# Optimization experiments

Hardware: AMD Instinct MI355X
Metric: run time of the kernel (lower is better)

## Reference

```python
import jax, jax.numpy as jnp
import numpy as np

IN_COUNT = 1024
OUT_COUNT = 1024
NUM_BASIS = 8
INPUT_ABS_MAX = 1.0
X_MIN = 0.0
X_MAX = 1.0
GAMMA_SCALE = 3.0
BATCH = 4096


def setup_inputs() -> dict:
    key = jax.random.key(0)
    k_x, k_c = jax.random.split(key)
    x = jax.random.normal(k_x, (BATCH, IN_COUNT), dtype=jnp.float32)
    coeffs = 0.01 * jax.random.normal(k_c, (OUT_COUNT, IN_COUNT, NUM_BASIS), dtype=jnp.float32)
    # fixed buffers
    centers_1d = jnp.linspace(X_MIN, X_MAX, NUM_BASIS)
    centers = jnp.broadcast_to(centers_1d[None, :], (IN_COUNT, NUM_BASIS)).astype(jnp.float32)
    delta = (X_MAX - X_MIN) / (NUM_BASIS - 1)
    gamma = GAMMA_SCALE / delta
    slopes = jnp.full((IN_COUNT, NUM_BASIS), gamma, dtype=jnp.float32)
    alpha = jnp.full((IN_COUNT,), (X_MAX - X_MIN) / (2.0 * INPUT_ABS_MAX), dtype=jnp.float32)
    beta = jnp.full((IN_COUNT,), 0.5 * (X_MIN + X_MAX), dtype=jnp.float32)
    return {"x": x, "coeffs": coeffs, "centers": centers, "slopes": slopes, "alpha": alpha, "beta": beta}


def reference(x, coeffs, centers, slopes, alpha, beta):
    # u: (B, in) affine transform with fixed alpha/beta
    u = alpha[None, :] * x + beta[None, :]
    # basis: (B, in, basis) = 0.5*(1+tanh(slope*(u - center)))
    basis = 0.5 * (1.0 + jnp.tanh(slopes[None, :, :] * (u[:, :, None] - centers[None, :, :])))
    # y[b,o] = sum_{i,m} coeffs[o,i,m] * basis[b,i,m]  (fused GEMM over in*basis)
    y = jnp.einsum('bim,oim->bo', basis, coeffs)
    return y
```

## Files before the change

kernel.cpp:

```cpp
#include <hip/hip_runtime.h>
#include <hip/hip_bf16.h>
#include <cstdint>
#include <cstddef>

#define BATCH 4096
#define INC   1024
#define OUTC  1024
#define NB    8
#define KDIM  (INC * NB)

#define BM 128
#define BN 128
#define BKB 128
#define SPLITS 3
#define GRID_BLOCKS ((OUTC / BN) * (BATCH / BM) * SPLITS)

#define EXPAND_BLOCKS  ((BATCH * INC) / 256)
#define QUANT_BLOCKS   OUTC
#define PREP_BLOCKS    (EXPAND_BLOCKS + QUANT_BLOCKS)

typedef int   v4i __attribute__((ext_vector_type(4)));
typedef char  v8c __attribute__((ext_vector_type(8)));
typedef short v8s __attribute__((ext_vector_type(8)));

__device__ __forceinline__ unsigned short f2bf(float f) {
  union { float f; unsigned u; } v; v.f = f;
  unsigned r = v.u + 0x7fffu + ((v.u >> 16) & 1u);
  return (unsigned short)(r >> 16);
}
__device__ __forceinline__ float bf2f(unsigned short h) {
  union { unsigned u; float f; } v; v.u = ((unsigned)h) << 16; return v.f;
}

__device__ __forceinline__ void gld16(const char* g, char* l) {
  __builtin_amdgcn_global_load_lds(
      (const __attribute__((address_space(1))) unsigned int*)g,
      (__attribute__((address_space(3))) unsigned int*)l, 16, 0, 0);
}

__global__ __launch_bounds__(256) void prep_kernel(
    const float* __restrict__ x, const float4* __restrict__ coeffs4,
    const float* __restrict__ centers, const float* __restrict__ slopes,
    const float* __restrict__ alpha, const float* __restrict__ beta,
    char* __restrict__ Ai8, int* __restrict__ Ci8i,
    float* __restrict__ maxrow, int* __restrict__ qcsum) {
  const int blk = blockIdx.x;
  const int tid = threadIdx.x;
  if (blk < EXPAND_BLOCKS) {
    const int idx = blk * 256 + tid;
    const int i = idx & (INC - 1);
    const float u = alpha[i] * x[idx] + beta[i];
    const float s0 = slopes[i * NB];
    const float c0 = centers[i * NB];
    const float c1 = centers[i * NB + 1];
    const float L2E2 = 2.8853900817779268f;
    const float a2 = L2E2 * s0;
    float e = __builtin_amdgcn_exp2f(a2 * (c0 - u));
    const float R = __builtin_amdgcn_exp2f(a2 * (c1 - c0));
    v8c q;
#pragma unroll
    for (int m = 0; m < 8; ++m) {
      float basis = __builtin_amdgcn_rcpf(1.0f + e);
      q[m] = (char)(int)rintf(basis * 254.0f - 127.0f);
      e *= R;
    }
    *(v8c*)(Ai8 + (size_t)idx * 8) = q;
  } else {
    const int o = blk - EXPAND_BLOCKS;
    const float4* row = coeffs4 + (size_t)o * (KDIM / 4);
    float4 v[8];
    float m = 0.0f;
#pragma unroll
    for (int j = 0; j < 8; ++j) {
      v[j] = row[tid + 256 * j];
      m = fmaxf(m, fmaxf(fmaxf(fabsf(v[j].x), fabsf(v[j].y)),
                         fmaxf(fabsf(v[j].z), fabsf(v[j].w))));
    }
#pragma unroll
    for (int off = 32; off; off >>= 1) m = fmaxf(m, __shfl_xor(m, off));
    __shared__ float wm[4];
    __shared__ int   wq[4];
    if ((tid & 63) == 0) wm[tid >> 6] = m;
    __syncthreads();
    const float M = fmaxf(fmaxf(fmaxf(wm[0], wm[1]), fmaxf(wm[2], wm[3])), 1e-30f);
    const float s = 127.0f / M;
    int qs = 0;
#pragma unroll
    for (int j = 0; j < 8; ++j) {
      int q0 = (int)rintf(v[j].x * s), q1 = (int)rintf(v[j].y * s);
      int q2 = (int)rintf(v[j].z * s), q3 = (int)rintf(v[j].w * s);
      Ci8i[(size_t)o * (KDIM / 4) + tid + 256 * j] =
          (q0 & 0xFF) | ((q1 & 0xFF) << 8) | ((q2 & 0xFF) << 16) | ((q3 & 0xFF) << 24);
      qs += q0 + q1 + q2 + q3;
    }
#pragma unroll
    for (int off = 32; off; off >>= 1) qs += __shfl_xor(qs, off);
    if ((tid & 63) == 0) wq[tid >> 6] = qs;
    __syncthreads();
    if (tid == 0) { maxrow[o] = M; qcsum[o] = wq[0] + wq[1] + wq[2] + wq[3]; }
  }
}

__global__ __launch_bounds__(256, 3) void gemm_kernel(
    const char* __restrict__ A, const char* __restrict__ C,
    unsigned short* __restrict__ partials) {
  __shared__ char As[BM * BKB];
  __shared__ char Bs[BN * BKB];

  const int id = (blockIdx.x & 7) * (GRID_BLOCKS / 8) + (blockIdx.x >> 3);
  const int z  = id >> 8;
  const int p  = id & 255;
  const int st = p >> 6;
  const int q  = p & 63;
  const int bx = q & 7;
  const int by = st * 8 + (q >> 3);
  const int bn0 = bx * BN;
  const int bm0 = by * BM;

  const int iters = (z == 0) ? 22 : 21;
  const int kt0   = (z == 0) ? 0 : (2816 + 2688 * (z - 1));

  const int tid  = threadIdx.x;
  const int wave = tid >> 6;
  const int lane = tid & 63;
  const int quad = lane >> 4;
  const int lm   = lane & 15;
  const int wm = (wave & 1) * 64;
  const int wn = (wave >> 1) * 64;
  unsigned short* out = partials + (size_t)z * BATCH * OUTC;

  const int r_in = lane >> 3;
  const int kg   = (lane & 7) ^ r_in;

  const char* pA[4];
  const char* pB[4];
  char* lA[4];
  char* lB[4];
#pragma unroll
  for (int j = 0; j < 4; ++j) {
    const int rb = wave * 32 + j * 8;
    pA[j] = A + (size_t)(bm0 + rb + r_in) * KDIM + kt0 + kg * 16;
    pB[j] = C + (size_t)(bn0 + rb + r_in) * KDIM + kt0 + kg * 16;
    lA[j] = As + rb * BKB;
    lB[j] = Bs + rb * BKB;
  }

  v4i acc[4][4] = {};

  for (int it = 0; it < iters; ++it) {
#pragma unroll
    for (int j = 0; j < 4; ++j) {
      gld16(pA[j], lA[j]);
      gld16(pB[j], lB[j]);
      pA[j] += BKB; pB[j] += BKB;
    }
    __syncthreads();

#pragma unroll
    for (int kp = 0; kp < 2; ++kp) {
      v4i a[4], b[4];
#pragma unroll
      for (int fm = 0; fm < 4; ++fm) {
        const int row = wm + fm * 16 + lm;
        const int kgs = (kp * 4 + quad) ^ (row & 7);
        a[fm] = *(const v4i*)(As + row * BKB + kgs * 16);
      }
#pragma unroll
      for (int fn = 0; fn < 4; ++fn) {
        const int row = wn + fn * 16 + lm;
        const int kgs = (kp * 4 + quad) ^ (row & 7);
        b[fn] = *(const v4i*)(Bs + row * BKB + kgs * 16);
      }
#pragma unroll
      for (int fm = 0; fm < 4; ++fm)
#pragma unroll
        for (int fn = 0; fn < 4; ++fn)
          acc[fm][fn] = __builtin_amdgcn_mfma_i32_16x16x64_i8(a[fm], b[fn], acc[fm][fn], 0, 0, 0);
    }
    __syncthreads();
  }

#pragma unroll
  for (int fm = 0; fm < 4; ++fm) {
    const int row0 = bm0 + wm + fm * 16 + quad * 4;
#pragma unroll
    for (int fn = 0; fn < 4; ++fn) {
      const int col = bn0 + wn + fn * 16 + lm;
#pragma unroll
      for (int r = 0; r < 4; ++r)
        out[(size_t)(row0 + r) * OUTC + col] = f2bf((float)acc[fm][fn][r]);
    }
  }
}

__global__ __launch_bounds__(256) void reduce_kernel(
    const unsigned short* __restrict__ P, const float* __restrict__ maxrow,
    const int* __restrict__ qcsum, float* __restrict__ out) {
  const size_t nel = (size_t)BATCH * OUTC;
  const size_t base = ((size_t)blockIdx.x * 256 + threadIdx.x) * 8;
  float s[8] = {};
#pragma unroll
  for (int t = 0; t < SPLITS; ++t) {
    v8s v = *(const v8s*)(P + t * nel + base);
#pragma unroll
    for (int j = 0; j < 8; ++j) s[j] += bf2f((unsigned short)v[j]);
  }
  const int o0 = (int)(base & (OUTC - 1));
  const float inv = 1.0f / 32258.0f;
#pragma unroll
  for (int j = 0; j < 8; ++j) {
    const float M = maxrow[o0 + j];
    const int   Q = qcsum[o0 + j];
    s[j] = M * (s[j] + 127.0f * (float)Q) * inv;
  }
  *(float4*)(out + base)     = float4{s[0], s[1], s[2], s[3]};
  *(float4*)(out + base + 4) = float4{s[4], s[5], s[6], s[7]};
}

extern "C" void kernel_launch(void* const* d_in, const int* in_sizes, int n_in,
                              void* d_out, int out_size, void* d_ws, size_t ws_size,
                              hipStream_t stream) {
  const float* x       = (const float*)d_in[0];
  const float* coeffs  = (const float*)d_in[1];
  const float* centers = (const float*)d_in[2];
  const float* slopes  = (const float*)d_in[3];
  const float* alpha   = (const float*)d_in[4];
  const float* beta    = (const float*)d_in[5];
  float* out = (float*)d_out;

  const size_t a_bytes    = (size_t)BATCH * KDIM;
  const size_t c_bytes    = (size_t)OUTC * KDIM;
  const size_t stat_bytes = OUTC * sizeof(float);
  const size_t qcs_bytes  = OUTC * sizeof(int);
  const size_t part_bytes = (size_t)SPLITS * BATCH * OUTC * 2;
  if (ws_size < a_bytes + c_bytes + stat_bytes + qcs_bytes + part_bytes) return;

  char*  Ai8    = (char*)d_ws;
  char*  Ci8    = Ai8 + a_bytes;
  float* maxrow = (float*)(Ci8 + c_bytes);
  int*   qcsum  = (int*)((char*)maxrow + stat_bytes);
  unsigned short* parts = (unsigned short*)((char*)qcsum + qcs_bytes);

  prep_kernel<<<PREP_BLOCKS, 256, 0, stream>>>(
      x, (const float4*)coeffs, centers, slopes, alpha, beta,
      Ai8, (int*)Ci8, maxrow, qcsum);

  gemm_kernel<<<GRID_BLOCKS, 256, 0, stream>>>(Ai8, Ci8, parts);

  reduce_kernel<<<(int)((size_t)BATCH * OUTC / 8 / 256), 256, 0, stream>>>(
      parts, maxrow, qcsum, out);
}
```

Before: 150.7 us.

## Use 256x256 double-buffered int8 GEMM tiles with 512 threads and 4 K-splits

Enlarges the GEMM tile to 256x256 with 8 waves, shrinks the K step to 64 bytes and double-buffers LDS so the next tile's global-to-LDS loads overlap the current MFMA work. It also adds s_setprio and s_barrier scheduling hints around the MFMA blocks and moves to 4 even K splits. The aim is more data reuse per LDS byte and hidden load latency. The cost is more partial-output traffic from the extra split, only 256 blocks total, and higher register pressure from 32 accumulators per wave.

```diff
diff --git a/kernel.cpp b/kernel.cpp
--- a/kernel.cpp
+++ b/kernel.cpp
@@ -9,10 +9,12 @@
 #define NB    8
 #define KDIM  (INC * NB)
 
-#define BM 128
-#define BN 128
-#define BKB 128
-#define SPLITS 3
+#define BM 256
+#define BN 256
+#define BKB 64
+#define SPLITS 4
+#define KZ (KDIM / SPLITS)
+#define KSTEPS (KZ / BKB)
 #define GRID_BLOCKS ((OUTC / BN) * (BATCH / BM) * SPLITS)
 
 #define EXPAND_BLOCKS  ((BATCH * INC) / 256)
@@ -101,87 +103,96 @@
   }
 }
 
-__global__ __launch_bounds__(256, 3) void gemm_kernel(
+__global__ __launch_bounds__(512, 2) void gemm_kernel(
     const char* __restrict__ A, const char* __restrict__ C,
     unsigned short* __restrict__ partials) {
-  __shared__ char As[BM * BKB];
-  __shared__ char Bs[BN * BKB];
+  __shared__ __align__(16) char As[2][BM * BKB];
+  __shared__ __align__(16) char Bs[2][BN * BKB];
 
   const int id = (blockIdx.x & 7) * (GRID_BLOCKS / 8) + (blockIdx.x >> 3);
-  const int z  = id >> 8;
-  const int p  = id & 255;
-  const int st = p >> 6;
-  const int q  = p & 63;
-  const int bx = q & 7;
-  const int by = st * 8 + (q >> 3);
+  const int z  = id >> 6;
+  const int p  = id & 63;
+  const int by = p >> 2;
+  const int bx = p & 3;
+  const int bm0 = by * BM;
   const int bn0 = bx * BN;
-  const int bm0 = by * BM;
-
-  const int iters = (z == 0) ? 22 : 21;
-  const int kt0   = (z == 0) ? 0 : (2816 + 2688 * (z - 1));
+  const int kt0 = z * KZ;
 
   const int tid  = threadIdx.x;
   const int wave = tid >> 6;
   const int lane = tid & 63;
   const int quad = lane >> 4;
   const int lm   = lane & 15;
-  const int wm = (wave & 1) * 64;
-  const int wn = (wave >> 1) * 64;
+  const int wm   = (wave >> 2) * 128;
+  const int wn   = (wave & 3) * 64;
+
+  const int r4 = lane >> 2;
+  const int gg = (lane & 3) ^ ((lane >> 3) & 3);
+
+  const char* pA0 = A + (size_t)(bm0 + wave * 32 + r4) * KDIM + kt0 + gg * 16;
+  const char* pB0 = C + (size_t)(bn0 + wave * 32 + r4) * KDIM + kt0 + gg * 16;
+  const int lo = wave * 32 * BKB;
+
+  v4i acc[8][4] = {};
+  const int kx = (quad ^ ((lm >> 1) & 3)) * 16;
+
+#define STAGE(sl)                                                        \
+  {                                                                      \
+    _Pragma("unroll")                                                    \
+    for (int j = 0; j < 2; ++j) {                                        \
+      gld16(pA0 + (size_t)j * (16 * KDIM), As[sl] + lo + j * (16 * BKB));\
+      gld16(pB0 + (size_t)j * (16 * KDIM), Bs[sl] + lo + j * (16 * BKB));\
+    }                                                                    \
+    pA0 += BKB; pB0 += BKB;                                              \
+  }
+
+  STAGE(0);
+  __syncthreads();
+
+  for (int t = 0; t < KSTEPS; ++t) {
+    const int cur = t & 1;
+
+    if (t + 1 < KSTEPS) STAGE(cur ^ 1);
+
+    const char* cA = As[cur];
+    const char* cB = Bs[cur];
+    v4i a[4], b[4];
+
+#pragma unroll
+    for (int f = 0; f < 4; ++f)
+      a[f] = *(const v4i*)(cA + (wm + f * 16 + lm) * BKB + kx);
+#pragma unroll
+    for (int f = 0; f < 4; ++f)
+      b[f] = *(const v4i*)(cB + (wn + f * 16 + lm) * BKB + kx);
+    __builtin_amdgcn_s_barrier();
+    __builtin_amdgcn_s_setprio(1);
+#pragma unroll
+    for (int fm = 0; fm < 4; ++fm)
+#pragma unroll
+      for (int fn = 0; fn < 4; ++fn)
+        acc[fm][fn] = __builtin_amdgcn_mfma_i32_16x16x64_i8(a[fm], b[fn], acc[fm][fn], 0, 0, 0);
+    __builtin_amdgcn_s_setprio(0);
+    __builtin_amdgcn_s_barrier();
+
+#pragma unroll
+    for (int f = 0; f < 4; ++f)
+      a[f] = *(const v4i*)(cA + (wm + (f + 4) * 16 + lm) * BKB + kx);
+    __builtin_amdgcn_s_barrier();
+    __builtin_amdgcn_s_setprio(1);
+#pragma unroll
+    for (int fm = 0; fm < 4; ++fm)
+#pragma unroll
+      for (int fn = 0; fn < 4; ++fn)
+        acc[fm + 4][fn] = __builtin_amdgcn_mfma_i32_16x16x64_i8(a[fm], b[fn], acc[fm + 4][fn], 0, 0, 0);
+    __builtin_amdgcn_s_setprio(0);
+
+    __syncthreads();
+  }
+#undef STAGE
+
   unsigned short* out = partials + (size_t)z * BATCH * OUTC;
-
-  const int r_in = lane >> 3;
-  const int kg   = (lane & 7) ^ r_in;
-
-  const char* pA[4];
-  const char* pB[4];
-  char* lA[4];
-  char* lB[4];
-#pragma unroll
-  for (int j = 0; j < 4; ++j) {
-    const int rb = wave * 32 + j * 8;
-    pA[j] = A + (size_t)(bm0 + rb + r_in) * KDIM + kt0 + kg * 16;
-    pB[j] = C + (size_t)(bn0 + rb + r_in) * KDIM + kt0 + kg * 16;
-    lA[j] = As + rb * BKB;
-    lB[j] = Bs + rb * BKB;
-  }
-
-  v4i acc[4][4] = {};
-
-  for (int it = 0; it < iters; ++it) {
-#pragma unroll
-    for (int j = 0; j < 4; ++j) {
-      gld16(pA[j], lA[j]);
-      gld16(pB[j], lB[j]);
-      pA[j] += BKB; pB[j] += BKB;
-    }
-    __syncthreads();
-
-#pragma unroll
-    for (int kp = 0; kp < 2; ++kp) {
-      v4i a[4], b[4];
-#pragma unroll
-      for (int fm = 0; fm < 4; ++fm) {
-        const int row = wm + fm * 16 + lm;
-        const int kgs = (kp * 4 + quad) ^ (row & 7);
-        a[fm] = *(const v4i*)(As + row * BKB + kgs * 16);
-      }
-#pragma unroll
-      for (int fn = 0; fn < 4; ++fn) {
-        const int row = wn + fn * 16 + lm;
-        const int kgs = (kp * 4 + quad) ^ (row & 7);
-        b[fn] = *(const v4i*)(Bs + row * BKB + kgs * 16);
-      }
-#pragma unroll
-      for (int fm = 0; fm < 4; ++fm)
-#pragma unroll
-        for (int fn = 0; fn < 4; ++fn)
-          acc[fm][fn] = __builtin_amdgcn_mfma_i32_16x16x64_i8(a[fm], b[fn], acc[fm][fn], 0, 0, 0);
-    }
-    __syncthreads();
-  }
-
-#pragma unroll
-  for (int fm = 0; fm < 4; ++fm) {
+#pragma unroll
+  for (int fm = 0; fm < 8; ++fm) {
     const int row0 = bm0 + wm + fm * 16 + quad * 4;
 #pragma unroll
     for (int fn = 0; fn < 4; ++fn) {
@@ -245,7 +256,7 @@
       x, (const float4*)coeffs, centers, slopes, alpha, beta,
       Ai8, (int*)Ci8, maxrow, qcsum);
 
-  gemm_kernel<<<GRID_BLOCKS, 256, 0, stream>>>(Ai8, Ci8, parts);
+  gemm_kernel<<<GRID_BLOCKS, 512, 0, stream>>>(Ai8, Ci8, parts);
 
   reduce_kernel<<<(int)((size_t)BATCH * OUTC / 8 / 256), 256, 0, stream>>>(
       parts, maxrow, qcsum, out);
```

New measurement: 164.2 us. 9.0% more time.
